# Kernel tuning notes

Measured on AMD Instinct MI355X. Metric: run time of the kernel, lower is better.

The kernel has to match this reference:

```python
import jax, jax.numpy as jnp
import numpy as np

N = 50000
E = 800000
IN_DIM = 128
HID_DIM = 128
OUT_DIM = 128
EPS = 1e-5


def setup_inputs() -> dict:
    key = jax.random.key(0)
    ks = jax.random.split(key, 6)
    x = jax.random.normal(ks[0], (N, IN_DIM), dtype=jnp.float32)
    src = jax.random.randint(ks[1], (E,), 0, N, dtype=jnp.int32)
    dst = jax.random.randint(ks[2], (E,), 0, N, dtype=jnp.int32)
    W1 = jax.random.normal(ks[3], (IN_DIM, HID_DIM), dtype=jnp.float32) / np.sqrt(IN_DIM)
    W2 = jax.random.normal(ks[4], (HID_DIM, OUT_DIM), dtype=jnp.float32) / np.sqrt(HID_DIM)
    return {
        "x": x, "src": src, "dst": dst,
        "W1": W1, "b1": jnp.zeros((HID_DIM,), jnp.float32),
        "gamma1": jnp.ones((HID_DIM,), jnp.float32), "beta1": jnp.zeros((HID_DIM,), jnp.float32),
        "W2": W2, "b2": jnp.zeros((OUT_DIM,), jnp.float32),
        "gamma2": jnp.ones((OUT_DIM,), jnp.float32), "beta2": jnp.zeros((OUT_DIM,), jnp.float32),
    }


def _degrees(src, dst, n):
    ones = jnp.ones(src.shape[0], jnp.float32)
    out_deg = jax.ops.segment_sum(ones, src, num_segments=n)
    in_deg = jax.ops.segment_sum(ones, dst, num_segments=n)
    # DGL norm='both' clamps degree to min 1 before pow(-0.5)
    return jnp.clip(out_deg, 1.0) ** -0.5, jnp.clip(in_deg, 1.0) ** -0.5


def _gconv(h, src, dst, d_out, d_in, W, b):
    h = h * d_out[:, None]                                   # [N, d] src-side norm
    m = jax.ops.segment_sum(h[src], dst, num_segments=h.shape[0])  # SpMM aggregate
    m = m * d_in[:, None]                                    # dst-side norm
    return m @ W + b


def _bn(h, gamma, beta):
    mu = jnp.mean(h, axis=0)
    var = jnp.var(h, axis=0)  # biased, matches torch BN training forward
    return gamma * (h - mu) * jax.lax.rsqrt(var + EPS) + beta


def reference(x, src, dst, W1, b1, gamma1, beta1, W2, b2, gamma2, beta2):
    d_out, d_in = _degrees(src, dst, x.shape[0])
    h1 = jax.nn.relu(_bn(_gconv(x, src, dst, d_out, d_in, W1, b1), gamma1, beta1))
    # dropout is identity in eval mode
    h2 = _bn(_gconv(h1, src, dst, d_out, d_in, W2, b2), gamma2, beta2)
    return jax.nn.relu(h2 + h1)
```

## Files before the change

### kernel.cpp

```cpp
#include <hip/hip_runtime.h>
#include <hip/hip_fp16.h>

#define NODES 50000
#define EDGES 800000
#define DIM 128
#define EPS_BN 1e-5f
#define SCAN_B 1024
#define SCAN_NB ((NODES + SCAN_B - 1) / SCAN_B)
#define GEMM_NB ((NODES + 63) / 64)
#define NCH 64
#define CHE (EDGES / NCH)
#define NR 4
#define RNG (NODES / NR)

typedef _Float16 half8 __attribute__((ext_vector_type(8)));
typedef float floatx4 __attribute__((ext_vector_type(4)));

union H8 { half8 v; __half2 h2[4]; };

__global__ __launch_bounds__(256) void hist_part_kernel(const int* __restrict__ src,
                                                        const int* __restrict__ dst,
                                                        unsigned short* __restrict__ Psrc,
                                                        unsigned short* __restrict__ Pdst) {
    __shared__ int h[RNG];
    int chunk = blockIdx.x & (NCH - 1);
    int range = blockIdx.x >> 6;
    const int* arr = blockIdx.y ? dst : src;
    unsigned short* P = blockIdx.y ? Pdst : Psrc;
    int base = range * RNG;
    for (int i = threadIdx.x; i < RNG; i += 256) h[i] = 0;
    __syncthreads();
    int e0 = chunk * CHE;
    for (int e = e0 + threadIdx.x; e < e0 + CHE; e += 256) {
        unsigned r = (unsigned)(arr[e] - base);
        if (r < (unsigned)RNG) atomicAdd(&h[r], 1);
    }
    __syncthreads();
    for (int i = threadIdx.x; i < RNG; i += 256)
        P[(size_t)chunk * NODES + base + i] = (unsigned short)h[i];
}

__global__ __launch_bounds__(256) void combine_kernel(const unsigned short* __restrict__ Psrc,
                                                      unsigned short* __restrict__ Pdst,
                                                      int* __restrict__ cnt_in,
                                                      float* __restrict__ dn_out,
                                                      float* __restrict__ sdeg,
                                                      float* __restrict__ dn_in) {
    int v = blockIdx.x * 256 + threadIdx.x;
    if (v >= NODES) return;
    int s = 0;
    #pragma unroll 8
    for (int j = 0; j < NCH; ++j) s += Psrc[(size_t)j * NODES + v];
    float fs = (float)max(s, 1);
    dn_out[v] = rsqrtf(fs);
    sdeg[v] = sqrtf(fs);
    int run = 0;
    #pragma unroll 8
    for (int j = 0; j < NCH; ++j) {
        int t = Pdst[(size_t)j * NODES + v];
        Pdst[(size_t)j * NODES + v] = (unsigned short)run;
        run += t;
    }
    cnt_in[v] = run;
    dn_in[v] = rsqrtf((float)max(run, 1));
}

__global__ __launch_bounds__(SCAN_B) void scan_p1_kernel(const int* __restrict__ cnt,
                                                         int* __restrict__ row_ptr,
                                                         int* __restrict__ blk_sums) {
    __shared__ int sm[SCAN_B];
    int t = threadIdx.x;
    int idx = blockIdx.x * SCAN_B + t;
    int v = (idx < NODES) ? cnt[idx] : 0;
    sm[t] = v;
    __syncthreads();
    #pragma unroll
    for (int off = 1; off < SCAN_B; off <<= 1) {
        int u = (t >= off) ? sm[t - off] : 0;
        __syncthreads();
        sm[t] += u;
        __syncthreads();
    }
    if (idx < NODES) row_ptr[idx] = sm[t] - v;
    if (t == SCAN_B - 1) blk_sums[blockIdx.x] = sm[t];
}

__global__ __launch_bounds__(SCAN_B) void scan_p3_kernel(int* __restrict__ row_ptr,
                                                         const int* __restrict__ blk_sums) {
    __shared__ int soff;
    int t = threadIdx.x;
    if (t < 64) {
        int v = (t < blockIdx.x) ? blk_sums[t] : 0;
        #pragma unroll
        for (int off = 32; off > 0; off >>= 1) v += __shfl_xor(v, off);
        if (t == 0) soff = v;
    }
    __syncthreads();
    int idx = blockIdx.x * SCAN_B + t;
    if (idx < NODES) row_ptr[idx] += soff;
    if (idx == 0) row_ptr[NODES] = EDGES;
}

__global__ __launch_bounds__(256) void fill_kernel(const int* __restrict__ src,
                                                   const int* __restrict__ dst,
                                                   const int* __restrict__ row_ptr,
                                                   const unsigned short* __restrict__ Pdst,
                                                   int* __restrict__ csr_src) {
    __shared__ int h[RNG];
    int chunk = blockIdx.x & (NCH - 1);
    int range = blockIdx.x >> 6;
    int base = range * RNG;
    for (int i = threadIdx.x; i < RNG; i += 256) h[i] = 0;
    __syncthreads();
    int e0 = chunk * CHE;
    const unsigned short* Pj = Pdst + (size_t)chunk * NODES;
    for (int e = e0 + threadIdx.x; e < e0 + CHE; e += 256) {
        int d = dst[e];
        unsigned r = (unsigned)(d - base);
        if (r < (unsigned)RNG) {
            int local = atomicAdd(&h[r], 1);
            csr_src[row_ptr[d] + (int)Pj[d] + local] = src[e];
        }
    }
}

__global__ __launch_bounds__(256) void w2h_kernel(const float* __restrict__ W1,
                                                  const float* __restrict__ W2,
                                                  __half* __restrict__ WhT1,
                                                  __half* __restrict__ WhT2,
                                                  float* __restrict__ p2) {
    int idx = blockIdx.x * 256 + threadIdx.x;
    if (blockIdx.x < 32) p2[blockIdx.x * 256 + threadIdx.x] = 0.f;
    const float* W = (idx < 16384) ? W1 : W2;
    __half* D = (idx < 16384) ? WhT1 : WhT2;
    int i = idx & 16383;
    int n = i >> 7;
    int k = i & 127;
    D[i] = __float2half(W[k * DIM + n]);
}

__global__ __launch_bounds__(256) void prescale_kernel(const float* __restrict__ x,
                                                       const float* __restrict__ dn_out,
                                                       __half* __restrict__ hs) {
    int idx = blockIdx.x * 256 + threadIdx.x;
    if (idx >= NODES * 16) return;
    int row = idx >> 4;
    int c8 = (idx & 15) * 8;
    float sc = dn_out[row];
    const float* xp = x + (size_t)row * DIM + c8;
    float4 v0 = *(const float4*)xp;
    float4 v1 = *(const float4*)(xp + 4);
    H8 u;
    u.h2[0] = __floats2half2_rn(v0.x * sc, v0.y * sc);
    u.h2[1] = __floats2half2_rn(v0.z * sc, v0.w * sc);
    u.h2[2] = __floats2half2_rn(v1.x * sc, v1.y * sc);
    u.h2[3] = __floats2half2_rn(v1.z * sc, v1.w * sc);
    *(half8*)((char*)hs + ((size_t)row * DIM + c8) * 2) = u.v;
}

__device__ __forceinline__ void acc_h8(half8 raw, float* a) {
    H8 u; u.v = raw;
    #pragma unroll
    for (int k = 0; k < 4; ++k) {
        float2 f = __half22float2(u.h2[k]);
        a[2 * k] += f.x;
        a[2 * k + 1] += f.y;
    }
}

__global__ __launch_bounds__(256) void pull_kernel(const __half* __restrict__ hs,
                                                   const int* __restrict__ row_ptr,
                                                   const int* __restrict__ csr_src,
                                                   const float* __restrict__ dn_in,
                                                   __half* __restrict__ agg) {
    int wid = threadIdx.x >> 6;
    int node = blockIdx.x * 4 + wid;
    if (node >= NODES) return;
    int lane = threadIdx.x & 63;
    int q = lane >> 4;
    int c = lane & 15;
    const char* base = (const char*)hs;
    int beg = row_ptr[node];
    int end = row_ptr[node + 1];
    float a[8];
    #pragma unroll
    for (int i = 0; i < 8; ++i) a[i] = 0.f;
    int eb = beg;
    for (; eb + 16 <= end; eb += 16) {
        int s0 = csr_src[eb + q];
        int s1 = csr_src[eb + 4 + q];
        int s2 = csr_src[eb + 8 + q];
        int s3 = csr_src[eb + 12 + q];
        half8 v0 = *(const half8*)(base + (size_t)s0 * 256 + c * 16);
        half8 v1 = *(const half8*)(base + (size_t)s1 * 256 + c * 16);
        half8 v2 = *(const half8*)(base + (size_t)s2 * 256 + c * 16);
        half8 v3 = *(const half8*)(base + (size_t)s3 * 256 + c * 16);
        acc_h8(v0, a);
        acc_h8(v1, a);
        acc_h8(v2, a);
        acc_h8(v3, a);
    }
    for (; eb + 8 <= end; eb += 8) {
        int s0 = csr_src[eb + q];
        int s1 = csr_src[eb + 4 + q];
        half8 v0 = *(const half8*)(base + (size_t)s0 * 256 + c * 16);
        half8 v1 = *(const half8*)(base + (size_t)s1 * 256 + c * 16);
        acc_h8(v0, a);
        acc_h8(v1, a);
    }
    for (; eb + 4 <= end; eb += 4) {
        int s0 = csr_src[eb + q];
        half8 v0 = *(const half8*)(base + (size_t)s0 * 256 + c * 16);
        acc_h8(v0, a);
    }
    if (eb + q < end) {
        int s0 = csr_src[eb + q];
        half8 v0 = *(const half8*)(base + (size_t)s0 * 256 + c * 16);
        acc_h8(v0, a);
    }
    #pragma unroll
    for (int i = 0; i < 8; ++i) a[i] += __shfl_xor(a[i], 32);
    #pragma unroll
    for (int i = 0; i < 8; ++i) a[i] += __shfl_xor(a[i], 16);
    if (lane < 16) {
        float sc = dn_in[node];
        H8 u;
        #pragma unroll
        for (int k = 0; k < 4; ++k)
            u.h2[k] = __floats2half2_rn(a[2 * k] * sc, a[2 * k + 1] * sc);
        *(half8*)((char*)agg + (size_t)node * 256 + c * 16) = u.v;
    }
}

__global__ __launch_bounds__(256) void gemm_mfma_kernel(const __half* __restrict__ A,
                                                        const __half* __restrict__ WhT,
                                                        const float* __restrict__ bias,
                                                        __half* __restrict__ hraw,
                                                        float* __restrict__ p2) {
    __shared__ float smem[8704];
    __half* wl = (__half*)smem;

    int t = threadIdx.x;

    #pragma unroll
    for (int i = 0; i < 8; ++i) {
        int cch = t + 256 * i;
        int n = cch >> 4;
        int ch = cch & 15;
        *(float4*)((char*)wl + n * 272 + ch * 16) =
            *(const float4*)((const char*)WhT + n * 256 + ch * 16);
    }

    int w = t >> 6;
    int lane = t & 63;
    int m = lane & 15;
    int quad = lane >> 4;
    int r0 = blockIdx.x * 64 + w * 16;
    int arow = r0 + m;

    half8 afrag[4];
    if (arow < NODES) {
        const char* ap = (const char*)(A + (size_t)arow * DIM);
        #pragma unroll
        for (int kt = 0; kt < 4; ++kt)
            afrag[kt] = *(const half8*)(ap + kt * 64 + quad * 16);
    } else {
        #pragma unroll
        for (int kt = 0; kt < 4; ++kt)
            #pragma unroll
            for (int j = 0; j < 8; ++j)
                afrag[kt][j] = (_Float16)0.0f;
    }

    floatx4 acc[8];
    floatx4 zf = {0.f, 0.f, 0.f, 0.f};
    #pragma unroll
    for (int ct = 0; ct < 8; ++ct) acc[ct] = zf;

    __syncthreads();

    #pragma unroll
    for (int kt = 0; kt < 4; ++kt) {
        #pragma unroll
        for (int ct = 0; ct < 8; ++ct) {
            half8 b = *(const half8*)((const char*)wl + (ct * 16 + m) * 272 + kt * 64 + quad * 16);
            acc[ct] = __builtin_amdgcn_mfma_f32_16x16x32_f16(afrag[kt], b, acc[ct], 0, 0, 0);
        }
    }

    __syncthreads();

    float* ps = smem;
    int g = w * 4 + quad;
    #pragma unroll
    for (int ct = 0; ct < 8; ++ct) {
        int col = ct * 16 + m;
        float bb = bias[col];
        float cs = 0.f, cq = 0.f;
        #pragma unroll
        for (int reg = 0; reg < 4; ++reg) {
            int row = r0 + quad * 4 + reg;
            if (row < NODES) {
                float o = acc[ct][reg] + bb;
                hraw[(size_t)row * DIM + col] = __float2half(o);
                cs += o;
                cq += o * o;
            }
        }
        ps[g * 128 + col] = cs;
        ps[2048 + g * 128 + col] = cq;
    }
    __syncthreads();

    float* pslot = p2 + (blockIdx.x & 31) * 256;
    if (t < 128) {
        float s = 0.f;
        #pragma unroll
        for (int gg = 0; gg < 16; ++gg) s += ps[gg * 128 + t];
        atomicAdd(pslot + t, s);
    } else {
        int cc = t - 128;
        float s = 0.f;
        #pragma unroll
        for (int gg = 0; gg < 16; ++gg) s += ps[2048 + gg * 128 + cc];
        atomicAdd(pslot + 128 + cc, s);
    }
}

__global__ __launch_bounds__(256) void stats_s2_kernel(float* __restrict__ p2,
                                                       float* __restrict__ stats) {
    int t = threadIdx.x;
    float s = 0.f;
    #pragma unroll
    for (int b = 0; b < 32; ++b) s += p2[b * 256 + t];
    stats[t] = s;
    #pragma unroll
    for (int b = 0; b < 32; ++b) p2[b * 256 + t] = 0.f;
}

__global__ __launch_bounds__(256) void bn_relu_scale_kernel(const __half* __restrict__ hraw,
                                                            __half* __restrict__ hs,
                                                            const float* __restrict__ stats,
                                                            const float* __restrict__ g,
                                                            const float* __restrict__ be,
                                                            const float* __restrict__ dn_out) {
    int idx = blockIdx.x * 256 + threadIdx.x;
    if (idx >= NODES * 16) return;
    int row = idx >> 4;
    int c8 = (idx & 15) * 8;
    const float invN = 1.0f / NODES;
    H8 u;
    u.v = *(const half8*)((const char*)hraw + ((size_t)row * DIM + c8) * 2);
    float o[8];
    #pragma unroll
    for (int k = 0; k < 4; ++k) {
        float2 f = __half22float2(u.h2[k]);
        o[2 * k] = f.x;
        o[2 * k + 1] = f.y;
    }
    #pragma unroll
    for (int j = 0; j < 8; ++j) {
        int cj = c8 + j;
        float mu = stats[cj] * invN;
        float var = stats[DIM + cj] * invN - mu * mu;
        float w = g[cj] * rsqrtf(var + EPS_BN);
        o[j] = fmaxf(w * (o[j] - mu) + be[cj], 0.f);
    }
    H8 us;
    float sc = dn_out[row];
    #pragma unroll
    for (int k = 0; k < 4; ++k)
        us.h2[k] = __floats2half2_rn(o[2 * k] * sc, o[2 * k + 1] * sc);
    *(half8*)((char*)hs + ((size_t)row * DIM + c8) * 2) = us.v;
}

__global__ __launch_bounds__(256) void bn_res_relu_kernel(const __half* __restrict__ hraw,
                                                          const __half* __restrict__ hs,
                                                          const float* __restrict__ sdeg,
                                                          float* __restrict__ out,
                                                          const float* __restrict__ stats,
                                                          const float* __restrict__ g,
                                                          const float* __restrict__ be) {
    int idx = blockIdx.x * 256 + threadIdx.x;
    if (idx >= NODES * 16) return;
    int row = idx >> 4;
    int c8 = (idx & 15) * 8;
    const float invN = 1.0f / NODES;
    float sd = sdeg[row];
    H8 u, ur;
    u.v = *(const half8*)((const char*)hraw + ((size_t)row * DIM + c8) * 2);
    ur.v = *(const half8*)((const char*)hs + ((size_t)row * DIM + c8) * 2);
    float o[8], r[8];
    #pragma unroll
    for (int k = 0; k < 4; ++k) {
        float2 f = __half22float2(u.h2[k]);
        float2 fr = __half22float2(ur.h2[k]);
        o[2 * k] = f.x; o[2 * k + 1] = f.y;
        r[2 * k] = fr.x * sd; r[2 * k + 1] = fr.y * sd;
    }
    #pragma unroll
    for (int j = 0; j < 8; ++j) {
        int cj = c8 + j;
        float mu = stats[cj] * invN;
        float var = stats[DIM + cj] * invN - mu * mu;
        float w = g[cj] * rsqrtf(var + EPS_BN);
        o[j] = fmaxf(w * (o[j] - mu) + be[cj] + r[j], 0.f);
    }
    float* op = out + (size_t)row * DIM + c8;
    float4 o0 = {o[0], o[1], o[2], o[3]};
    float4 o1 = {o[4], o[5], o[6], o[7]};
    *(float4*)op = o0;
    *(float4*)(op + 4) = o1;
}

extern "C" void kernel_launch(void* const* d_in, const int* in_sizes, int n_in,
                              void* d_out, int out_size, void* d_ws, size_t ws_size,
                              hipStream_t stream) {
    const float* x      = (const float*)d_in[0];
    const int*   src    = (const int*)d_in[1];
    const int*   dst    = (const int*)d_in[2];
    const float* W1     = (const float*)d_in[3];
    const float* b1     = (const float*)d_in[4];
    const float* gamma1 = (const float*)d_in[5];
    const float* beta1  = (const float*)d_in[6];
    const float* W2     = (const float*)d_in[7];
    const float* b2     = (const float*)d_in[8];
    const float* gamma2 = (const float*)d_in[9];
    const float* beta2  = (const float*)d_in[10];
    float* out = (float*)d_out;

    char* wsc = (char*)d_ws;
    int*   cnt_in   = (int*)wsc;                     wsc += NODES * 4;
    float* dn_out   = (float*)wsc;                   wsc += NODES * 4;
    float* sdeg     = (float*)wsc;                   wsc += NODES * 4;
    float* dn_in    = (float*)wsc;                   wsc += NODES * 4;
    int*   row_ptr  = (int*)wsc;                     wsc += (NODES + 1) * 4;
    int*   csr_src  = (int*)wsc;                     wsc += EDGES * 4;
    float* stats    = (float*)wsc;                   wsc += 2 * DIM * 4;
    int*   blk_sums = (int*)wsc;                     wsc += 64 * 4;
    __half* WhT1    = (__half*)wsc;                  wsc += DIM * DIM * 2;
    __half* WhT2    = (__half*)wsc;                  wsc += DIM * DIM * 2;
    float* p2       = (float*)wsc;                   wsc += 32 * 256 * 4;
    unsigned short* Psrc = (unsigned short*)wsc;     wsc += (size_t)NCH * NODES * 2;
    unsigned short* Pdst = (unsigned short*)wsc;     wsc += (size_t)NCH * NODES * 2;
    __half* hs      = (__half*)wsc;                  wsc += (size_t)NODES * DIM * 2;
    __half* agg     = (__half*)wsc;                  wsc += (size_t)NODES * DIM * 2;
    __half* hraw    = (__half*)wsc;                  wsc += (size_t)NODES * DIM * 2;

    const int T = 256;
    const int grid_pull = (NODES + 3) / 4;
    const int grid_e16  = (NODES * 16 + T - 1) / T;

    hist_part_kernel<<<dim3(NR * NCH, 2), T, 0, stream>>>(src, dst, Psrc, Pdst);
    combine_kernel<<<(NODES + T - 1) / T, T, 0, stream>>>(Psrc, Pdst, cnt_in, dn_out, sdeg, dn_in);
    scan_p1_kernel<<<SCAN_NB, SCAN_B, 0, stream>>>(cnt_in, row_ptr, blk_sums);
    scan_p3_kernel<<<SCAN_NB, SCAN_B, 0, stream>>>(row_ptr, blk_sums);
    fill_kernel<<<NR * NCH, T, 0, stream>>>(src, dst, row_ptr, Pdst, csr_src);

    w2h_kernel<<<128, T, 0, stream>>>(W1, W2, WhT1, WhT2, p2);

    prescale_kernel<<<grid_e16, T, 0, stream>>>(x, dn_out, hs);
    pull_kernel<<<grid_pull, T, 0, stream>>>(hs, row_ptr, csr_src, dn_in, agg);
    gemm_mfma_kernel<<<GEMM_NB, T, 0, stream>>>(agg, WhT1, b1, hraw, p2);
    stats_s2_kernel<<<1, T, 0, stream>>>(p2, stats);
    bn_relu_scale_kernel<<<grid_e16, T, 0, stream>>>(hraw, hs, stats, gamma1, beta1, dn_out);

    pull_kernel<<<grid_pull, T, 0, stream>>>(hs, row_ptr, csr_src, dn_in, agg);
    gemm_mfma_kernel<<<GEMM_NB, T, 0, stream>>>(agg, WhT2, b2, hraw, p2);
    stats_s2_kernel<<<1, T, 0, stream>>>(p2, stats);
    bn_res_relu_kernel<<<grid_e16, T, 0, stream>>>(hraw, hs, sdeg, out, stats, gamma2, beta2);
}
```

Baseline: 276.1 us.

## Build CSR with global atomics instead of partitioned shared-memory histograms

The degree counting and CSR fill now use global atomicAdd on per-node counters and a cursor array. This replaces the chunked shared-memory histograms, the 64-way partial-count combine pass and the rank-based fill. Weight conversion and counter zeroing are folded into one init kernel. The aim is to cut the repeated edge scans and the large partial-count traffic. The cost is global atomic contention and a nondeterministic neighbour order within each CSR row, which can change fp16 accumulation order slightly.

```diff
diff --git a/kernel.cpp b/kernel.cpp
--- a/kernel.cpp
+++ b/kernel.cpp
@@ -8,61 +8,59 @@
 #define SCAN_B 1024
 #define SCAN_NB ((NODES + SCAN_B - 1) / SCAN_B)
 #define GEMM_NB ((NODES + 63) / 64)
-#define NCH 64
-#define CHE (EDGES / NCH)
-#define NR 4
-#define RNG (NODES / NR)
+#define PRE_NB ((NODES * 16) / 256)
+#define EDGE_NB ((EDGES + 255) / 256)
 
 typedef _Float16 half8 __attribute__((ext_vector_type(8)));
 typedef float floatx4 __attribute__((ext_vector_type(4)));
 
 union H8 { half8 v; __half2 h2[4]; };
 
-__global__ __launch_bounds__(256) void hist_part_kernel(const int* __restrict__ src,
-                                                        const int* __restrict__ dst,
-                                                        unsigned short* __restrict__ Psrc,
-                                                        unsigned short* __restrict__ Pdst) {
-    __shared__ int h[RNG];
-    int chunk = blockIdx.x & (NCH - 1);
-    int range = blockIdx.x >> 6;
-    const int* arr = blockIdx.y ? dst : src;
-    unsigned short* P = blockIdx.y ? Pdst : Psrc;
-    int base = range * RNG;
-    for (int i = threadIdx.x; i < RNG; i += 256) h[i] = 0;
-    __syncthreads();
-    int e0 = chunk * CHE;
-    for (int e = e0 + threadIdx.x; e < e0 + CHE; e += 256) {
-        unsigned r = (unsigned)(arr[e] - base);
-        if (r < (unsigned)RNG) atomicAdd(&h[r], 1);
-    }
-    __syncthreads();
-    for (int i = threadIdx.x; i < RNG; i += 256)
-        P[(size_t)chunk * NODES + base + i] = (unsigned short)h[i];
-}
-
-__global__ __launch_bounds__(256) void combine_kernel(const unsigned short* __restrict__ Psrc,
-                                                      unsigned short* __restrict__ Pdst,
-                                                      int* __restrict__ cnt_in,
-                                                      float* __restrict__ dn_out,
-                                                      float* __restrict__ sdeg,
-                                                      float* __restrict__ dn_in) {
+__global__ __launch_bounds__(256) void init_kernel(const float* __restrict__ W1,
+                                                   const float* __restrict__ W2,
+                                                   __half* __restrict__ WhT1,
+                                                   __half* __restrict__ WhT2,
+                                                   float* __restrict__ p2,
+                                                   int* __restrict__ cnt2) {
+    int b = blockIdx.x;
+    int t = threadIdx.x;
+    if (b < 128) {
+        int idx = b * 256 + t;
+        if (b < 32) p2[b * 256 + t] = 0.f;
+        const float* W = (idx < 16384) ? W1 : W2;
+        __half* D = (idx < 16384) ? WhT1 : WhT2;
+        int i = idx & 16383;
+        int n = i >> 7;
+        int k = i & 127;
+        D[i] = __float2half(W[k * DIM + n]);
+    } else {
+        int idx = (b - 128) * 256 + t;
+        if (idx < 2 * NODES) cnt2[idx] = 0;
+    }
+}
+
+__global__ __launch_bounds__(256) void deg_kernel(const int* __restrict__ src,
+                                                  const int* __restrict__ dst,
+                                                  int* __restrict__ cnt_out,
+                                                  int* __restrict__ cnt_in) {
+    int e = blockIdx.x * 256 + threadIdx.x;
+    if (e < EDGES) {
+        atomicAdd(&cnt_out[src[e]], 1);
+        atomicAdd(&cnt_in[dst[e]], 1);
+    }
+}
+
+__global__ __launch_bounds__(256) void norm_kernel(const int* __restrict__ cnt_out,
+                                                   const int* __restrict__ cnt_in,
+                                                   float* __restrict__ dn_out,
+                                                   float* __restrict__ sdeg,
+                                                   float* __restrict__ dn_in) {
     int v = blockIdx.x * 256 + threadIdx.x;
     if (v >= NODES) return;
-    int s = 0;
-    #pragma unroll 8
-    for (int j = 0; j < NCH; ++j) s += Psrc[(size_t)j * NODES + v];
-    float fs = (float)max(s, 1);
+    float fs = (float)max(cnt_out[v], 1);
     dn_out[v] = rsqrtf(fs);
     sdeg[v] = sqrtf(fs);
-    int run = 0;
-    #pragma unroll 8
-    for (int j = 0; j < NCH; ++j) {
-        int t = Pdst[(size_t)j * NODES + v];
-        Pdst[(size_t)j * NODES + v] = (unsigned short)run;
-        run += t;
-    }
-    cnt_in[v] = run;
-    dn_in[v] = rsqrtf((float)max(run, 1));
+    dn_in[v] = rsqrtf((float)max(cnt_in[v], 1));
 }
 
 __global__ __launch_bounds__(SCAN_B) void scan_p1_kernel(const int* __restrict__ cnt,
@@ -86,7 +84,8 @@
 }
 
 __global__ __launch_bounds__(SCAN_B) void scan_p3_kernel(int* __restrict__ row_ptr,
-                                                         const int* __restrict__ blk_sums) {
+                                                         const int* __restrict__ blk_sums,
+                                                         int* __restrict__ cursor) {
     __shared__ int soff;
     int t = threadIdx.x;
     if (t < 64) {
@@ -97,46 +96,23 @@
     }
     __syncthreads();
     int idx = blockIdx.x * SCAN_B + t;
-    if (idx < NODES) row_ptr[idx] += soff;
+    if (idx < NODES) {
+        int v = row_ptr[idx] + soff;
+        row_ptr[idx] = v;
+        cursor[idx] = v;
+    }
     if (idx == 0) row_ptr[NODES] = EDGES;
 }
 
-__global__ __launch_bounds__(256) void fill_kernel(const int* __restrict__ src,
-                                                   const int* __restrict__ dst,
-                                                   const int* __restrict__ row_ptr,
-                                                   const unsigned short* __restrict__ Pdst,
-                                                   int* __restrict__ csr_src) {
-    __shared__ int h[RNG];
-    int chunk = blockIdx.x & (NCH - 1);
-    int range = blockIdx.x >> 6;
-    int base = range * RNG;
-    for (int i = threadIdx.x; i < RNG; i += 256) h[i] = 0;
-    __syncthreads();
-    int e0 = chunk * CHE;
-    const unsigned short* Pj = Pdst + (size_t)chunk * NODES;
-    for (int e = e0 + threadIdx.x; e < e0 + CHE; e += 256) {
-        int d = dst[e];
-        unsigned r = (unsigned)(d - base);
-        if (r < (unsigned)RNG) {
-            int local = atomicAdd(&h[r], 1);
-            csr_src[row_ptr[d] + (int)Pj[d] + local] = src[e];
-        }
-    }
-}
-
-__global__ __launch_bounds__(256) void w2h_kernel(const float* __restrict__ W1,
-                                                  const float* __restrict__ W2,
-                                                  __half* __restrict__ WhT1,
-                                                  __half* __restrict__ WhT2,
-                                                  float* __restrict__ p2) {
-    int idx = blockIdx.x * 256 + threadIdx.x;
-    if (blockIdx.x < 32) p2[blockIdx.x * 256 + threadIdx.x] = 0.f;
-    const float* W = (idx < 16384) ? W1 : W2;
-    __half* D = (idx < 16384) ? WhT1 : WhT2;
-    int i = idx & 16383;
-    int n = i >> 7;
-    int k = i & 127;
-    D[i] = __float2half(W[k * DIM + n]);
+__global__ __launch_bounds__(256) void fill_atomic_kernel(const int* __restrict__ src,
+                                                          const int* __restrict__ dst,
+                                                          int* __restrict__ cursor,
+                                                          int* __restrict__ csr_src) {
+    int e = blockIdx.x * 256 + threadIdx.x;
+    if (e < EDGES) {
+        int pos = atomicAdd(&cursor[dst[e]], 1);
+        csr_src[pos] = src[e];
+    }
 }
 
 __global__ __launch_bounds__(256) void prescale_kernel(const float* __restrict__ x,
@@ -430,19 +406,19 @@
     float* out = (float*)d_out;
 
     char* wsc = (char*)d_ws;
+    int*   cnt_out  = (int*)wsc;                     wsc += NODES * 4;
     int*   cnt_in   = (int*)wsc;                     wsc += NODES * 4;
     float* dn_out   = (float*)wsc;                   wsc += NODES * 4;
     float* sdeg     = (float*)wsc;                   wsc += NODES * 4;
     float* dn_in    = (float*)wsc;                   wsc += NODES * 4;
     int*   row_ptr  = (int*)wsc;                     wsc += (NODES + 1) * 4;
+    int*   cursor   = (int*)wsc;                     wsc += NODES * 4;
     int*   csr_src  = (int*)wsc;                     wsc += EDGES * 4;
     float* stats    = (float*)wsc;                   wsc += 2 * DIM * 4;
     int*   blk_sums = (int*)wsc;                     wsc += 64 * 4;
     __half* WhT1    = (__half*)wsc;                  wsc += DIM * DIM * 2;
     __half* WhT2    = (__half*)wsc;                  wsc += DIM * DIM * 2;
     float* p2       = (float*)wsc;                   wsc += 32 * 256 * 4;
-    unsigned short* Psrc = (unsigned short*)wsc;     wsc += (size_t)NCH * NODES * 2;
-    unsigned short* Pdst = (unsigned short*)wsc;     wsc += (size_t)NCH * NODES * 2;
     __half* hs      = (__half*)wsc;                  wsc += (size_t)NODES * DIM * 2;
     __half* agg     = (__half*)wsc;                  wsc += (size_t)NODES * DIM * 2;
     __half* hraw    = (__half*)wsc;                  wsc += (size_t)NODES * DIM * 2;
@@ -450,14 +426,14 @@
     const int T = 256;
     const int grid_pull = (NODES + 3) / 4;
     const int grid_e16  = (NODES * 16 + T - 1) / T;
-
-    hist_part_kernel<<<dim3(NR * NCH, 2), T, 0, stream>>>(src, dst, Psrc, Pdst);
-    combine_kernel<<<(NODES + T - 1) / T, T, 0, stream>>>(Psrc, Pdst, cnt_in, dn_out, sdeg, dn_in);
+    const int grid_init = 128 + (2 * NODES + T - 1) / T;
+
+    init_kernel<<<grid_init, T, 0, stream>>>(W1, W2, WhT1, WhT2, p2, cnt_out);
+    deg_kernel<<<EDGE_NB, T, 0, stream>>>(src, dst, cnt_out, cnt_in);
+    norm_kernel<<<(NODES + T - 1) / T, T, 0, stream>>>(cnt_out, cnt_in, dn_out, sdeg, dn_in);
     scan_p1_kernel<<<SCAN_NB, SCAN_B, 0, stream>>>(cnt_in, row_ptr, blk_sums);
-    scan_p3_kernel<<<SCAN_NB, SCAN_B, 0, stream>>>(row_ptr, blk_sums);
-    fill_kernel<<<NR * NCH, T, 0, stream>>>(src, dst, row_ptr, Pdst, csr_src);
-
-    w2h_kernel<<<128, T, 0, stream>>>(W1, W2, WhT1, WhT2, p2);
+    scan_p3_kernel<<<SCAN_NB, SCAN_B, 0, stream>>>(row_ptr, blk_sums, cursor);
+    fill_atomic_kernel<<<EDGE_NB, T, 0, stream>>>(src, dst, cursor, csr_src);
 
     prescale_kernel<<<grid_e16, T, 0, stream>>>(x, dn_out, hs);
     pull_kernel<<<grid_pull, T, 0, stream>>>(hs, row_ptr, csr_src, dn_in, agg);
```

Result: slower. 338.2 us (+22.5%).
